# Optimization experiments

Measured on AMD Instinct MI355X. Metric: run time of the kernel, lower is better.

The kernel has to match this reference:

```python
import jax, jax.numpy as jnp
import numpy as np

B, C, H, W = 4, 512, 64, 64
C8 = C // 8


def setup_inputs() -> dict:
    key = jax.random.key(0)
    ks = jax.random.split(key, 5)
    s1 = 1.0 / np.sqrt(C)
    return {
        "feat_map": jax.random.normal(ks[0], (B, C, H, W), jnp.float32),
        "w1": jax.random.normal(ks[1], (C8, C), jnp.float32) * s1,
        "b1": jnp.zeros((C8,), jnp.float32),
        "w2": jax.random.normal(ks[2], (C8, C), jnp.float32) * s1,
        "b2": jnp.zeros((C8,), jnp.float32),
        "w3": jax.random.normal(ks[3], (C, C), jnp.float32) * s1,
        "b3": jnp.zeros((C,), jnp.float32),
        "gamma": jax.random.normal(ks[4], (1,), jnp.float32) * 0.1,
    }


def reference(feat_map, w1, b1, w2, b2, w3, b3, gamma):
    b, c, h, w = feat_map.shape
    n = h * w
    x = feat_map.reshape(b, c, n)  # [B,C,N]
    # 1x1 convs are channel-mixing GEMMs
    q = jnp.einsum('kc,bcn->bnk', w1, x) + b1[None, None, :]   # [B,N,C8]
    k = jnp.einsum('kc,bcn->bkn', w2, x) + b2[None, :, None]   # [B,C8,N]
    v = jnp.einsum('dc,bcn->bdn', w3, x) + b3[None, :, None]   # [B,C,N]
    relation = jnp.einsum('bik,bkj->bij', q, k)                # [B,N,N]
    attn = jax.nn.softmax(relation, axis=-1)                   # softmax over keys j
    # feat_refine[b,c,i] = sum_j v[b,c,j] * attn[b,i,j]
    refine = jnp.einsum('bdj,bij->bdi', v, attn)               # [B,C,N]
    out = gamma[0] * refine.reshape(b, c, h, w) + feat_map
    return out
```

## Files before the change

kernel.cpp:

```cpp
#include <hip/hip_runtime.h>
#include <hip/hip_bf16.h>

typedef __attribute__((ext_vector_type(8))) short bf16x8_t;
typedef __attribute__((ext_vector_type(4))) float f32x4_t;

#define B_   4
#define C_   512
#define N_   4096
#define NQK_ 128
#define NT_  128
#define NP_  64

typedef unsigned short ushort_t;

__device__ __forceinline__ ushort_t f2bf(float f) {
    union { float f; unsigned int u; } un; un.f = f;
    unsigned int r = un.u + 0x7FFF + ((un.u >> 16) & 1);
    return (ushort_t)(r >> 16);
}

__device__ __forceinline__ bf16x8_t load8(const ushort_t* p) {
    return *reinterpret_cast<const bf16x8_t*>(p);
}

__device__ __forceinline__ unsigned pk2(float lo, float hi) {
    return (unsigned)f2bf(lo) | ((unsigned)f2bf(hi) << 16);
}

#define GLL16(g, l) __builtin_amdgcn_global_load_lds( \
    (const __attribute__((address_space(1))) unsigned int*)(g), \
    (__attribute__((address_space(3))) unsigned int*)(l), 16, 0, 0)

__global__ __launch_bounds__(256) void transpose_cast_x(
        const float* __restrict__ x, ushort_t* __restrict__ Xt,
        const float* __restrict__ w1, const float* __restrict__ b1,
        const float* __restrict__ w2, const float* __restrict__ b2,
        const float* __restrict__ w3, const float* __restrict__ b3,
        ushort_t* __restrict__ Wb, float* __restrict__ bias_all) {
    if (blockIdx.z == 4) {
        int bid = blockIdx.y * 64 + blockIdx.x;
        int t0 = bid * 256 + threadIdx.x;
        for (int idx = t0; idx < 640 * 512 + 640; idx += 131072) {
            if (idx < 64 * 512) {
                Wb[idx] = f2bf(w1[idx]);
            } else if (idx < 128 * 512) {
                Wb[idx] = f2bf(w2[idx - 64 * 512]);
            } else if (idx < 640 * 512) {
                Wb[idx] = f2bf(w3[idx - 128 * 512]);
            } else {
                int i = idx - 640 * 512;
                bias_all[i] = (i < 64) ? b1[i] : (i < 128 ? b2[i - 64] : b3[i - 128]);
            }
        }
        return;
    }
    int b = blockIdx.z, c0 = blockIdx.y * 64, n0 = blockIdx.x * 64;
    int tid = threadIdx.x;
    __shared__ float t[64][65];
    const float* xb = x + ((size_t)b * C_ + c0) * N_ + n0;
    #pragma unroll
    for (int it = 0; it < 4; ++it) {
        int cl = it * 16 + (tid >> 4), nq = (tid & 15) * 4;
        const float4 v = *reinterpret_cast<const float4*>(xb + (size_t)cl * N_ + nq);
        t[cl][nq + 0] = v.x; t[cl][nq + 1] = v.y;
        t[cl][nq + 2] = v.z; t[cl][nq + 3] = v.w;
    }
    __syncthreads();
    #pragma unroll
    for (int it = 0; it < 4; ++it) {
        int nl = it * 16 + (tid >> 4), cq = (tid & 15) * 4;
        ushort4 o;
        o.x = f2bf(t[cq + 0][nl]); o.y = f2bf(t[cq + 1][nl]);
        o.z = f2bf(t[cq + 2][nl]); o.w = f2bf(t[cq + 3][nl]);
        *reinterpret_cast<ushort4*>(&Xt[((size_t)b * N_ + n0 + nl) * C_ + c0 + cq]) = o;
    }
}

__global__ __launch_bounds__(256) void gemm_qkv_kernel(
        const ushort_t* __restrict__ Xt, const ushort_t* __restrict__ Wb,
        const float* __restrict__ bias, ushort_t* __restrict__ QK,
        ushort_t* __restrict__ V) {
    __shared__ ushort_t Al[2][4096];
    __shared__ ushort_t Bl[2][4096];
    int sel = blockIdx.y;
    int n0 = blockIdx.x * 128;
    int tid = threadIdx.x;
    int l = tid & 63, w = tid >> 6;
    int wr = w >> 1, wc = w & 1;
    int lr = l & 15, lg = l >> 4;

    int m0 = 0, bV = 0;
    const ushort_t* asrc;
    const ushort_t* bsrc;
    if (sel < 4) {
        asrc = Xt + ((size_t)sel * N_ + n0) * 512;
        bsrc = Wb;
    } else {
        m0 = ((sel - 4) & 3) * 128;
        bV = (sel - 4) >> 2;
        asrc = Wb + (size_t)(128 + m0) * 512;
        bsrc = Xt + ((size_t)bV * N_ + n0) * 512;
    }
    const ushort_t* ast = asrc + (size_t)(l >> 2) * 512 + (l & 3) * 8;
    const ushort_t* bst = bsrc + (size_t)(l >> 2) * 512 + (l & 3) * 8;

#define STAGEK(BUF, K0)                                                        \
    {                                                                          \
        GLL16(ast + (size_t)(w * 32) * 512 + (K0),      &Al[BUF][w * 1024]);       \
        GLL16(ast + (size_t)(w * 32 + 16) * 512 + (K0), &Al[BUF][w * 1024 + 512]); \
        GLL16(bst + (size_t)(w * 32) * 512 + (K0),      &Bl[BUF][w * 1024]);       \
        GLL16(bst + (size_t)(w * 32 + 16) * 512 + (K0), &Bl[BUF][w * 1024 + 512]); \
    }

    f32x4_t acc[4][4] = {};
    STAGEK(0, 0)
    for (int i = 0; i < 16; ++i) {
        int cur = i & 1;
        if (i < 15) {
            STAGEK(cur ^ 1, (i + 1) * 32)
            asm volatile("s_waitcnt vmcnt(4)" ::: "memory");
        } else {
            asm volatile("s_waitcnt vmcnt(0)" ::: "memory");
        }
        asm volatile("" ::: "memory");
        __builtin_amdgcn_s_barrier();
        asm volatile("" ::: "memory");
        bf16x8_t a[4], b8[4];
        #pragma unroll
        for (int f = 0; f < 4; ++f) {
            a[f]  = load8(&Al[cur][(wr * 64 + f * 16 + lr) * 32 + lg * 8]);
            b8[f] = load8(&Bl[cur][(wc * 64 + f * 16 + lr) * 32 + lg * 8]);
        }
        #pragma unroll
        for (int fi = 0; fi < 4; ++fi)
            #pragma unroll
            for (int fj = 0; fj < 4; ++fj)
                acc[fi][fj] = __builtin_amdgcn_mfma_f32_16x16x32_bf16(
                    a[fi], b8[fj], acc[fi][fj], 0, 0, 0);
        asm volatile("" ::: "memory");
        __builtin_amdgcn_s_barrier();
        asm volatile("" ::: "memory");
    }
#undef STAGEK

    if (sel < 4) {
        #pragma unroll
        for (int fi = 0; fi < 4; ++fi)
            #pragma unroll
            for (int fj = 0; fj < 4; ++fj)
                #pragma unroll
                for (int r = 0; r < 4; ++r) {
                    int n = n0 + wr * 64 + fi * 16 + lg * 4 + r;
                    int col = wc * 64 + fj * 16 + lr;
                    QK[((size_t)sel * N_ + n) * NQK_ + col] = f2bf(acc[fi][fj][r] + bias[col]);
                }
    } else {
        #pragma unroll
        for (int fi = 0; fi < 4; ++fi)
            #pragma unroll
            for (int fj = 0; fj < 4; ++fj)
                #pragma unroll
                for (int r = 0; r < 4; ++r) {
                    int d = m0 + wr * 64 + fi * 16 + lg * 4 + r;
                    int n = n0 + wc * 64 + fj * 16 + lr;
                    V[((size_t)bV * C_ + d) * N_ + n] = f2bf(acc[fi][fj][r] + bias[128 + d]);
                }
    }
}

__global__ __launch_bounds__(768, 3) void attn_kernel(
        const ushort_t* __restrict__ QK, const ushort_t* __restrict__ V,
        const float* __restrict__ feat, const float* __restrict__ gamma,
        float* __restrict__ out) {
    __shared__ ushort_t Vl[3][16384];
    __shared__ ushort_t Kl3[3][4096];
    __shared__ ushort_t Pl[2][4096];
    __shared__ float    fl[2][128];
    __shared__ __align__(16) unsigned flagl[2][8];
    __shared__ float    invl[64];

    int bid = blockIdx.x;
    int lid = (bid & 7) * 32 + (bid >> 3);
    int b  = lid >> 6;
    int i0 = (lid & 63) * 64;

    int tid = threadIdx.x;
    int l = tid & 63, w = tid >> 6;
    int lr = l & 15, lg = l >> 4;
    int ds = (w >= 4) ? (w - 4) : 0;

    const ushort_t* QKb = QK + (size_t)b * N_ * NQK_;
    const ushort_t* Vb  = V  + (size_t)b * C_ * N_;

    bf16x8_t qf0 = {}, qf1 = {};
    const ushort_t* ksrc = nullptr;
    float mreg = -1e30f, ssum = 0.0f;
    const int maskk = (lr & 7) << 4;
    if (w < 4) {
        qf0 = load8(QKb + (size_t)(i0 + w * 16 + lr) * NQK_ + lg * 8);
        qf1 = load8(QKb + (size_t)(i0 + w * 16 + lr) * NQK_ + 32 + lg * 8);
        int p = w * 1024 + l * 16;
        int o = p ^ (((p >> 7) & 7) << 4);
        ksrc = QKb + (size_t)(o >> 7) * NQK_ + 64 + ((o & 127) >> 1);
    }

    int cst = (l & 7) ^ (l >> 3);
    const ushort_t* vsrc = Vb + (size_t)(ds * 64 + 2 * (l >> 3) + (cst >> 2)) * N_
                              + (cst & 3) * 8;
    int c2 = ((lr & 1) * 4 + lg) ^ (lr >> 1);
    const int vread = ds * 2048 + (lr >> 1) * 64 + c2 * 8;
    f32x4_t acc[4][4] = {};

    if (w < 4) {
        GLL16(ksrc,                         &Kl3[0][w * 512]);
        GLL16(ksrc + (size_t)1 * 32 * NQK_, &Kl3[0][2048 + w * 512]);
        GLL16(ksrc + (size_t)2 * 32 * NQK_, &Kl3[1][w * 512]);
        GLL16(ksrc + (size_t)3 * 32 * NQK_, &Kl3[1][2048 + w * 512]);
        asm volatile("s_waitcnt vmcnt(2)" ::: "memory");
    } else {
        #pragma unroll
        for (int h = 0; h < 4; ++h)
            GLL16(vsrc + (size_t)h * 16 * N_,      &Vl[0][ds * 2048 + h * 512]);
        #pragma unroll
        for (int h = 0; h < 4; ++h)
            GLL16(vsrc + (size_t)h * 16 * N_ + 32, &Vl[1][ds * 2048 + h * 512]);
        #pragma unroll
        for (int h = 0; h < 4; ++h)
            GLL16(vsrc + (size_t)h * 16 * N_ + 64, &Vl[2][ds * 2048 + h * 512]);
    }
    asm volatile("" ::: "memory");
    __builtin_amdgcn_s_barrier();
    asm volatile("" ::: "memory");

#define SOFTMAX_WRITE(SO0, SO1, PM, TT)                                        \
    {                                                                          \
        float pmax = fmaxf(fmaxf(fmaxf(SO0[0],SO0[1]), fmaxf(SO0[2],SO0[3])),  \
                           fmaxf(fmaxf(SO1[0],SO1[1]), fmaxf(SO1[2],SO1[3]))); \
        pmax = fmaxf(pmax, __shfl_xor(pmax, 16));                              \
        pmax = fmaxf(pmax, __shfl_xor(pmax, 32));                              \
        bool anyneed = __any(pmax > mreg + 8.0f);                              \
        if (anyneed) {                                                         \
            float mn = fmaxf(mreg, pmax);                                      \
            float f_ = __expf(mreg - mn);                                      \
            mreg = mn; ssum *= f_;                                             \
            if (lg == 0) fl[PM][(TT) * 64 + w * 16 + lr] = f_;                 \
        }                                                                      \
        if (l == 0) flagl[PM][(TT) * 4 + w] = anyneed ? 1u : 0u;               \
        float e00 = __expf(SO0[0]-mreg), e01 = __expf(SO0[1]-mreg);            \
        float e02 = __expf(SO0[2]-mreg), e03 = __expf(SO0[3]-mreg);            \
        float e10 = __expf(SO1[0]-mreg), e11 = __expf(SO1[1]-mreg);            \
        float e12 = __expf(SO1[2]-mreg), e13 = __expf(SO1[3]-mreg);            \
        ssum += (e00+e01)+(e02+e03)+(e10+e11)+(e12+e13);    \
        int lt = lr + (lg >> 1) * 16;                                          \
        uint2 w0v; w0v.x = pk2(e00, e01); w0v.y = pk2(e02, e03);               \
        uint2 w1v; w1v.x = pk2(e10, e11); w1v.y = pk2(e12, e13);               \
        *reinterpret_cast<uint2*>(&Pl[PM][(TT)*2048 + w*512 + lt*8 + (lg&1)*4]) = w0v; \
        *reinterpret_cast<uint2*>(&Pl[PM][(TT)*2048 + w*512 + (lt+32)*8 + (lg&1)*4]) = w1v; \
    }

#define PVSTEP(PB, TT, VB, STJ, DOSTAGE)                                       \
    {                                                                          \
        bf16x8_t vf[4];                                                        \
        _Pragma("unroll") for (int dt = 0; dt < 4; ++dt)                       \
            vf[dt] = load8(&Vl[VB][vread + dt * 512]);                         \
        asm volatile("s_waitcnt lgkmcnt(0)" ::: "memory");                     \
        if (DOSTAGE) {                                                         \
            const ushort_t* vsT = vsrc + (STJ) * 32;                           \
            _Pragma("unroll") for (int h = 0; h < 4; ++h)                      \
                GLL16(vsT + (size_t)h * 16 * N_, &Vl[VB][ds * 2048 + h * 512]); \
        }                                                                      \
        uint4 fv = *reinterpret_cast<const uint4*>(&flagl[PB][(TT) * 4]);      \
        if ((int)__builtin_amdgcn_readfirstlane(fv.x)) {                       \
            float fq = fl[PB][(TT) * 64 + lr];                                 \
            _Pragma("unroll") for (int dt = 0; dt < 4; ++dt) acc[dt][0] *= fq; \
        }                                                                      \
        if ((int)__builtin_amdgcn_readfirstlane(fv.y)) {                       \
            float fq = fl[PB][(TT) * 64 + 16 + lr];                            \
            _Pragma("unroll") for (int dt = 0; dt < 4; ++dt) acc[dt][1] *= fq; \
        }                                                                      \
        if ((int)__builtin_amdgcn_readfirstlane(fv.z)) {                       \
            float fq = fl[PB][(TT) * 64 + 32 + lr];                            \
            _Pragma("unroll") for (int dt = 0; dt < 4; ++dt) acc[dt][2] *= fq; \
        }                                                                      \
        if ((int)__builtin_amdgcn_readfirstlane(fv.w)) {                       \
            float fq = fl[PB][(TT) * 64 + 48 + lr];                            \
            _Pragma("unroll") for (int dt = 0; dt < 4; ++dt) acc[dt][3] *= fq; \
        }                                                                      \
        __builtin_amdgcn_s_setprio(1);                                         \
        _Pragma("unroll") for (int qt = 0; qt < 4; ++qt) {                     \
            bf16x8_t pa = load8(&Pl[PB][(TT) * 2048 + qt * 512 + l * 8]);      \
            _Pragma("unroll") for (int dt = 0; dt < 4; ++dt)                   \
                acc[dt][qt] = __builtin_amdgcn_mfma_f32_16x16x32_bf16(         \
                    vf[dt], pa, acc[dt][qt], 0, 0, 0);                         \
        }                                                                      \
        __builtin_amdgcn_s_setprio(0);                                         \
    }

    for (int p = 0; p < NP_; ++p) {
        int pb = p % 3;
        if (w < 4) {
            if (p + 2 < NP_) {
                int pn = pb + 2; if (pn >= 3) pn -= 3;
                GLL16(ksrc + (size_t)(2 * p + 4) * 32 * NQK_, &Kl3[pn][w * 512]);
                GLL16(ksrc + (size_t)(2 * p + 5) * 32 * NQK_, &Kl3[pn][2048 + w * 512]);
            }
            const ushort_t* kbp = &Kl3[pb][0];
            bf16x8_t kf00, kf01, kf10, kf11;
            { int o = (lr << 7) + (lg << 4);              kf00 = load8(kbp + ((o ^ maskk) >> 1)); }
            { int o = (lr << 7) + 64 + (lg << 4);         kf01 = load8(kbp + ((o ^ maskk) >> 1)); }
            { int o = ((16 + lr) << 7) + (lg << 4);       kf10 = load8(kbp + ((o ^ maskk) >> 1)); }
            { int o = ((16 + lr) << 7) + 64 + (lg << 4);  kf11 = load8(kbp + ((o ^ maskk) >> 1)); }
            f32x4_t s00 = {0.f,0.f,0.f,0.f}, s01 = {0.f,0.f,0.f,0.f};
            s00 = __builtin_amdgcn_mfma_f32_16x16x32_bf16(kf00, qf0, s00, 0,0,0);
            s00 = __builtin_amdgcn_mfma_f32_16x16x32_bf16(kf01, qf1, s00, 0,0,0);
            s01 = __builtin_amdgcn_mfma_f32_16x16x32_bf16(kf10, qf0, s01, 0,0,0);
            s01 = __builtin_amdgcn_mfma_f32_16x16x32_bf16(kf11, qf1, s01, 0,0,0);
            const ushort_t* kbq = kbp + 2048;
            bf16x8_t kg00, kg01, kg10, kg11;
            { int o = (lr << 7) + (lg << 4);              kg00 = load8(kbq + ((o ^ maskk) >> 1)); }
            { int o = (lr << 7) + 64 + (lg << 4);         kg01 = load8(kbq + ((o ^ maskk) >> 1)); }
            { int o = ((16 + lr) << 7) + (lg << 4);       kg10 = load8(kbq + ((o ^ maskk) >> 1)); }
            { int o = ((16 + lr) << 7) + 64 + (lg << 4);  kg11 = load8(kbq + ((o ^ maskk) >> 1)); }
            f32x4_t s10 = {0.f,0.f,0.f,0.f}, s11 = {0.f,0.f,0.f,0.f};
            s10 = __builtin_amdgcn_mfma_f32_16x16x32_bf16(kg00, qf0, s10, 0,0,0);
            s10 = __builtin_amdgcn_mfma_f32_16x16x32_bf16(kg01, qf1, s10, 0,0,0);
            s11 = __builtin_amdgcn_mfma_f32_16x16x32_bf16(kg10, qf0, s11, 0,0,0);
            s11 = __builtin_amdgcn_mfma_f32_16x16x32_bf16(kg11, qf1, s11, 0,0,0);
            int bank = p & 1;
            SOFTMAX_WRITE(s00, s01, bank, 0)
            SOFTMAX_WRITE(s10, s11, bank, 1)
            asm volatile("s_waitcnt vmcnt(2) lgkmcnt(0)" ::: "memory");
        } else {
            if (p >= 1) {
                int pbk = (p - 1) & 1;
                int j0 = 2 * p - 2, j1 = 2 * p - 1;
                PVSTEP(pbk, 0, j0 % 3, j0 + 3, (j0 + 3 < NT_))
                PVSTEP(pbk, 1, j1 % 3, j1 + 3, (j1 + 3 < NT_))
            }
            asm volatile("s_waitcnt vmcnt(4)" ::: "memory");
        }
        asm volatile("" ::: "memory");
        __builtin_amdgcn_s_barrier();
        asm volatile("" ::: "memory");
    }

    if (w < 4) {
        ssum += __shfl_xor(ssum, 16);
        ssum += __shfl_xor(ssum, 32);
        if (lg == 0) invl[w * 16 + lr] = 1.0f / ssum;
        asm volatile("s_waitcnt lgkmcnt(0)" ::: "memory");
    } else {
        asm volatile("s_waitcnt vmcnt(0)" ::: "memory");
    }
    asm volatile("" ::: "memory");
    __builtin_amdgcn_s_barrier();
    asm volatile("" ::: "memory");

    if (w >= 4) {
        PVSTEP(1, 0, 0, 0, false)
        PVSTEP(1, 1, 1, 0, false)
        asm volatile("s_waitcnt lgkmcnt(0)" ::: "memory");

        float g = gamma[0];
        float iq0 = invl[lr], iq1 = invl[16 + lr], iq2 = invl[32 + lr], iq3 = invl[48 + lr];
        #pragma unroll
        for (int dt = 0; dt < 4; ++dt) {
            #pragma unroll
            for (int r = 0; r < 4; ++r) {
                size_t row = ((size_t)b * C_ + ds * 64 + dt * 16 + lg * 4 + r) * N_;
                size_t i0r = row + i0;
                { size_t idx = i0r + lr;      out[idx] = g * acc[dt][0][r] * iq0 + feat[idx]; }
                { size_t idx = i0r + 16 + lr; out[idx] = g * acc[dt][1][r] * iq1 + feat[idx]; }
                { size_t idx = i0r + 32 + lr; out[idx] = g * acc[dt][2][r] * iq2 + feat[idx]; }
                { size_t idx = i0r + 48 + lr; out[idx] = g * acc[dt][3][r] * iq3 + feat[idx]; }
            }
        }
    }
#undef PVSTEP
#undef SOFTMAX_WRITE
}

extern "C" void kernel_launch(void* const* d_in, const int* in_sizes, int n_in,
                              void* d_out, int out_size, void* d_ws, size_t ws_size,
                              hipStream_t stream) {
    const float* feat  = (const float*)d_in[0];
    const float* w1    = (const float*)d_in[1];
    const float* b1    = (const float*)d_in[2];
    const float* w2    = (const float*)d_in[3];
    const float* b2    = (const float*)d_in[4];
    const float* w3    = (const float*)d_in[5];
    const float* b3    = (const float*)d_in[6];
    const float* gamma = (const float*)d_in[7];
    float* out = (float*)d_out;

    char* ws = (char*)d_ws;
    ushort_t* Xt      = (ushort_t*)(ws);
    ushort_t* Wb      = (ushort_t*)(ws + 16777216);
    float*    biasAll = (float*)   (ws + 17432576);
    ushort_t* QKp     = (ushort_t*)(ws + 17435136);
    ushort_t* Vp      = (ushort_t*)(ws + 21629440);
    if (ws_size < 38406656) return;

    hipLaunchKernelGGL(transpose_cast_x, dim3(64, 8, 5), dim3(256), 0, stream,
                       feat, Xt, w1, b1, w2, b2, w3, b3, Wb, biasAll);
    hipLaunchKernelGGL(gemm_qkv_kernel, dim3(32, 20), dim3(256), 0, stream,
                       Xt, Wb, biasAll, QKp, Vp);
    hipLaunchKernelGGL(attn_kernel, dim3(256), dim3(768), 0, stream,
                       QKp, Vp, feat, gamma, out);
}
```

Baseline: 139.7 us.

## Split PV work across softmax waves and shrink QKV GEMM tiles for more blocks

In the attention kernel, the four softmax waves now also take part in the P·V product: each covers 32 value channels (2 tiles), while the four PV waves drop from 64 to 48 channels (3 tiles). This spreads the MFMA load over all eight waves instead of leaving the softmax waves idle during PV, at the cost of extra vmcnt bookkeeping and more V staging traffic on the softmax waves. Separately, the QKV GEMM tile is halved along M (64 rows per block), raising the grid from 640 to 1280 blocks with a 1D index for better CU occupancy. The trade-off is lower per-block data reuse.

```diff
diff --git a/kernel.cpp b/kernel.cpp
--- a/kernel.cpp
+++ b/kernel.cpp
@@ -80,59 +80,60 @@
         const ushort_t* __restrict__ Xt, const ushort_t* __restrict__ Wb,
         const float* __restrict__ bias, ushort_t* __restrict__ QK,
         ushort_t* __restrict__ V) {
-    __shared__ ushort_t Al[2][4096];
+    __shared__ ushort_t Al[2][2048];
     __shared__ ushort_t Bl[2][4096];
-    int sel = blockIdx.y;
-    int n0 = blockIdx.x * 128;
+    int bid = blockIdx.x;
     int tid = threadIdx.x;
     int l = tid & 63, w = tid >> 6;
     int wr = w >> 1, wc = w & 1;
     int lr = l & 15, lg = l >> 4;
 
-    int m0 = 0, bV = 0;
+    int b, n0, d0 = 0;
+    bool isQK = (bid < 256);
     const ushort_t* asrc;
     const ushort_t* bsrc;
-    if (sel < 4) {
-        asrc = Xt + ((size_t)sel * N_ + n0) * 512;
+    if (isQK) {
+        b = bid >> 6; n0 = (bid & 63) * 64;
+        asrc = Xt + ((size_t)b * N_ + n0) * 512;
         bsrc = Wb;
     } else {
-        m0 = ((sel - 4) & 3) * 128;
-        bV = (sel - 4) >> 2;
-        asrc = Wb + (size_t)(128 + m0) * 512;
-        bsrc = Xt + ((size_t)bV * N_ + n0) * 512;
+        int v = bid - 256;
+        b = v >> 8; d0 = ((v >> 5) & 7) * 64; n0 = (v & 31) * 128;
+        asrc = Wb + (size_t)(128 + d0) * 512;
+        bsrc = Xt + ((size_t)b * N_ + n0) * 512;
     }
     const ushort_t* ast = asrc + (size_t)(l >> 2) * 512 + (l & 3) * 8;
     const ushort_t* bst = bsrc + (size_t)(l >> 2) * 512 + (l & 3) * 8;
 
-#define STAGEK(BUF, K0)                                                        \
-    {                                                                          \
-        GLL16(ast + (size_t)(w * 32) * 512 + (K0),      &Al[BUF][w * 1024]);       \
-        GLL16(ast + (size_t)(w * 32 + 16) * 512 + (K0), &Al[BUF][w * 1024 + 512]); \
-        GLL16(bst + (size_t)(w * 32) * 512 + (K0),      &Bl[BUF][w * 1024]);       \
+#define STAGEK(BUF, K0)                                                          \
+    {                                                                            \
+        GLL16(ast + (size_t)(w * 16) * 512 + (K0),      &Al[BUF][w * 512]);      \
+        GLL16(bst + (size_t)(w * 32) * 512 + (K0),      &Bl[BUF][w * 1024]);     \
         GLL16(bst + (size_t)(w * 32 + 16) * 512 + (K0), &Bl[BUF][w * 1024 + 512]); \
     }
 
-    f32x4_t acc[4][4] = {};
+    f32x4_t acc[2][4] = {};
     STAGEK(0, 0)
     for (int i = 0; i < 16; ++i) {
         int cur = i & 1;
         if (i < 15) {
             STAGEK(cur ^ 1, (i + 1) * 32)
-            asm volatile("s_waitcnt vmcnt(4)" ::: "memory");
+            asm volatile("s_waitcnt vmcnt(3)" ::: "memory");
         } else {
             asm volatile("s_waitcnt vmcnt(0)" ::: "memory");
         }
         asm volatile("" ::: "memory");
         __builtin_amdgcn_s_barrier();
         asm volatile("" ::: "memory");
-        bf16x8_t a[4], b8[4];
-        #pragma unroll
-        for (int f = 0; f < 4; ++f) {
-            a[f]  = load8(&Al[cur][(wr * 64 + f * 16 + lr) * 32 + lg * 8]);
+        bf16x8_t a[2], b8[4];
+        #pragma unroll
+        for (int f = 0; f < 2; ++f)
+            a[f]  = load8(&Al[cur][(wr * 32 + f * 16 + lr) * 32 + lg * 8]);
+        #pragma unroll
+        for (int f = 0; f < 4; ++f)
             b8[f] = load8(&Bl[cur][(wc * 64 + f * 16 + lr) * 32 + lg * 8]);
-        }
-        #pragma unroll
-        for (int fi = 0; fi < 4; ++fi)
+        #pragma unroll
+        for (int fi = 0; fi < 2; ++fi)
             #pragma unroll
             for (int fj = 0; fj < 4; ++fj)
                 acc[fi][fj] = __builtin_amdgcn_mfma_f32_16x16x32_bf16(
@@ -143,27 +144,27 @@
     }
 #undef STAGEK
 
-    if (sel < 4) {
-        #pragma unroll
-        for (int fi = 0; fi < 4; ++fi)
+    if (isQK) {
+        #pragma unroll
+        for (int fi = 0; fi < 2; ++fi)
             #pragma unroll
             for (int fj = 0; fj < 4; ++fj)
                 #pragma unroll
                 for (int r = 0; r < 4; ++r) {
-                    int n = n0 + wr * 64 + fi * 16 + lg * 4 + r;
+                    int n = n0 + wr * 32 + fi * 16 + lg * 4 + r;
                     int col = wc * 64 + fj * 16 + lr;
-                    QK[((size_t)sel * N_ + n) * NQK_ + col] = f2bf(acc[fi][fj][r] + bias[col]);
+                    QK[((size_t)b * N_ + n) * NQK_ + col] = f2bf(acc[fi][fj][r] + bias[col]);
                 }
     } else {
         #pragma unroll
-        for (int fi = 0; fi < 4; ++fi)
+        for (int fi = 0; fi < 2; ++fi)
             #pragma unroll
             for (int fj = 0; fj < 4; ++fj)
                 #pragma unroll
                 for (int r = 0; r < 4; ++r) {
-                    int d = m0 + wr * 64 + fi * 16 + lg * 4 + r;
+                    int d = d0 + wr * 32 + fi * 16 + lg * 4 + r;
                     int n = n0 + wc * 64 + fj * 16 + lr;
-                    V[((size_t)bV * C_ + d) * N_ + n] = f2bf(acc[fi][fj][r] + bias[128 + d]);
+                    V[((size_t)b * C_ + d) * N_ + n] = f2bf(acc[fi][fj][r] + bias[128 + d]);
                 }
     }
 }
@@ -187,7 +188,8 @@
     int tid = threadIdx.x;
     int l = tid & 63, w = tid >> 6;
     int lr = l & 15, lg = l >> 4;
-    int ds = (w >= 4) ? (w - 4) : 0;
+
+    int chbase = (w < 4) ? (384 + w * 32) : ((w - 4) * 48);
 
     const ushort_t* QKb = QK + (size_t)b * N_ * NQK_;
     const ushort_t* Vb  = V  + (size_t)b * C_ * N_;
@@ -205,28 +207,30 @@
     }
 
     int cst = (l & 7) ^ (l >> 3);
-    const ushort_t* vsrc = Vb + (size_t)(ds * 64 + 2 * (l >> 3) + (cst >> 2)) * N_
+    const ushort_t* vsrc = Vb + (size_t)(chbase + 2 * (l >> 3) + (cst >> 2)) * N_
                               + (cst & 3) * 8;
     int c2 = ((lr & 1) * 4 + lg) ^ (lr >> 1);
-    const int vread = ds * 2048 + (lr >> 1) * 64 + c2 * 8;
-    f32x4_t acc[4][4] = {};
+    const int vread = chbase * 32 + (lr >> 1) * 64 + c2 * 8;
+    f32x4_t acc[3][4] = {};
 
     if (w < 4) {
         GLL16(ksrc,                         &Kl3[0][w * 512]);
         GLL16(ksrc + (size_t)1 * 32 * NQK_, &Kl3[0][2048 + w * 512]);
         GLL16(ksrc + (size_t)2 * 32 * NQK_, &Kl3[1][w * 512]);
         GLL16(ksrc + (size_t)3 * 32 * NQK_, &Kl3[1][2048 + w * 512]);
-        asm volatile("s_waitcnt vmcnt(2)" ::: "memory");
+        #pragma unroll
+        for (int j = 0; j < 3; ++j)
+            #pragma unroll
+            for (int h = 0; h < 2; ++h)
+                GLL16(vsrc + (size_t)h * 16 * N_ + j * 32,
+                      &Vl[j][chbase * 32 + h * 512]);
     } else {
         #pragma unroll
-        for (int h = 0; h < 4; ++h)
-            GLL16(vsrc + (size_t)h * 16 * N_,      &Vl[0][ds * 2048 + h * 512]);
-        #pragma unroll
-        for (int h = 0; h < 4; ++h)
-            GLL16(vsrc + (size_t)h * 16 * N_ + 32, &Vl[1][ds * 2048 + h * 512]);
-        #pragma unroll
-        for (int h = 0; h < 4; ++h)
-            GLL16(vsrc + (size_t)h * 16 * N_ + 64, &Vl[2][ds * 2048 + h * 512]);
+        for (int j = 0; j < 3; ++j)
+            #pragma unroll
+            for (int h = 0; h < 3; ++h)
+                GLL16(vsrc + (size_t)h * 16 * N_ + j * 32,
+                      &Vl[j][chbase * 32 + h * 512]);
     }
     asm volatile("" ::: "memory");
     __builtin_amdgcn_s_barrier();
@@ -258,38 +262,38 @@
         *reinterpret_cast<uint2*>(&Pl[PM][(TT)*2048 + w*512 + (lt+32)*8 + (lg&1)*4]) = w1v; \
     }
 
-#define PVSTEP(PB, TT, VB, STJ, DOSTAGE)                                       \
+#define PVSTEP(PB, TT, VB, STJ, DOSTAGE, DTN, NGL)                             \
     {                                                                          \
-        bf16x8_t vf[4];                                                        \
-        _Pragma("unroll") for (int dt = 0; dt < 4; ++dt)                       \
+        bf16x8_t vf[3];                                                        \
+        _Pragma("unroll") for (int dt = 0; dt < (DTN); ++dt)                   \
             vf[dt] = load8(&Vl[VB][vread + dt * 512]);                         \
         asm volatile("s_waitcnt lgkmcnt(0)" ::: "memory");                     \
         if (DOSTAGE) {                                                         \
             const ushort_t* vsT = vsrc + (STJ) * 32;                           \
-            _Pragma("unroll") for (int h = 0; h < 4; ++h)                      \
-                GLL16(vsT + (size_t)h * 16 * N_, &Vl[VB][ds * 2048 + h * 512]); \
+            _Pragma("unroll") for (int h = 0; h < (NGL); ++h)                  \
+                GLL16(vsT + (size_t)h * 16 * N_, &Vl[VB][chbase * 32 + h * 512]); \
         }                                                                      \
         uint4 fv = *reinterpret_cast<const uint4*>(&flagl[PB][(TT) * 4]);      \
         if ((int)__builtin_amdgcn_readfirstlane(fv.x)) {                       \
             float fq = fl[PB][(TT) * 64 + lr];                                 \
-            _Pragma("unroll") for (int dt = 0; dt < 4; ++dt) acc[dt][0] *= fq; \
+            _Pragma("unroll") for (int dt = 0; dt < (DTN); ++dt) acc[dt][0] *= fq; \
         }                                                                      \
         if ((int)__builtin_amdgcn_readfirstlane(fv.y)) {                       \
             float fq = fl[PB][(TT) * 64 + 16 + lr];                            \
-            _Pragma("unroll") for (int dt = 0; dt < 4; ++dt) acc[dt][1] *= fq; \
+            _Pragma("unroll") for (int dt = 0; dt < (DTN); ++dt) acc[dt][1] *= fq; \
         }                                                                      \
         if ((int)__builtin_amdgcn_readfirstlane(fv.z)) {                       \
             float fq = fl[PB][(TT) * 64 + 32 + lr];                            \
-            _Pragma("unroll") for (int dt = 0; dt < 4; ++dt) acc[dt][2] *= fq; \
+            _Pragma("unroll") for (int dt = 0; dt < (DTN); ++dt) acc[dt][2] *= fq; \
         }                                                                      \
         if ((int)__builtin_amdgcn_readfirstlane(fv.w)) {                       \
             float fq = fl[PB][(TT) * 64 + 48 + lr];                            \
-            _Pragma("unroll") for (int dt = 0; dt < 4; ++dt) acc[dt][3] *= fq; \
+            _Pragma("unroll") for (int dt = 0; dt < (DTN); ++dt) acc[dt][3] *= fq; \
         }                                                                      \
         __builtin_amdgcn_s_setprio(1);                                         \
         _Pragma("unroll") for (int qt = 0; qt < 4; ++qt) {                     \
             bf16x8_t pa = load8(&Pl[PB][(TT) * 2048 + qt * 512 + l * 8]);      \
-            _Pragma("unroll") for (int dt = 0; dt < 4; ++dt)                   \
+            _Pragma("unroll") for (int dt = 0; dt < (DTN); ++dt)               \
                 acc[dt][qt] = __builtin_amdgcn_mfma_f32_16x16x32_bf16(         \
                     vf[dt], pa, acc[dt][qt], 0, 0, 0);                         \
         }                                                                      \
@@ -299,6 +303,7 @@
     for (int p = 0; p < NP_; ++p) {
         int pb = p % 3;
         if (w < 4) {
+            asm volatile("s_waitcnt vmcnt(6)" ::: "memory");
             if (p + 2 < NP_) {
                 int pn = pb + 2; if (pn >= 3) pn -= 3;
                 GLL16(ksrc + (size_t)(2 * p + 4) * 32 * NQK_, &Kl3[pn][w * 512]);
@@ -329,15 +334,25 @@
             int bank = p & 1;
             SOFTMAX_WRITE(s00, s01, bank, 0)
             SOFTMAX_WRITE(s10, s11, bank, 1)
-            asm volatile("s_waitcnt vmcnt(2) lgkmcnt(0)" ::: "memory");
+            if (p >= 1) {
+                int pbk = (p - 1) & 1;
+                int j0 = 2 * p - 2, j1 = 2 * p - 1;
+                if (p < 62) { asm volatile("s_waitcnt vmcnt(4)" ::: "memory"); }
+                else        { asm volatile("s_waitcnt vmcnt(2)" ::: "memory"); }
+                PVSTEP(pbk, 0, j0 % 3, j0 + 3, (j0 + 3 < NT_), 2, 2)
+                if (p < 62) { asm volatile("s_waitcnt vmcnt(4)" ::: "memory"); }
+                else        { asm volatile("s_waitcnt vmcnt(2)" ::: "memory"); }
+                PVSTEP(pbk, 1, j1 % 3, j1 + 3, (j1 + 3 < NT_), 2, 2)
+            }
+            asm volatile("s_waitcnt lgkmcnt(0)" ::: "memory");
         } else {
             if (p >= 1) {
                 int pbk = (p - 1) & 1;
                 int j0 = 2 * p - 2, j1 = 2 * p - 1;
-                PVSTEP(pbk, 0, j0 % 3, j0 + 3, (j0 + 3 < NT_))
-                PVSTEP(pbk, 1, j1 % 3, j1 + 3, (j1 + 3 < NT_))
+                PVSTEP(pbk, 0, j0 % 3, j0 + 3, (j0 + 3 < NT_), 3, 3)
+                PVSTEP(pbk, 1, j1 % 3, j1 + 3, (j1 + 3 < NT_), 3, 3)
             }
-            asm volatile("s_waitcnt vmcnt(4)" ::: "memory");
+            asm volatile("s_waitcnt vmcnt(3)" ::: "memory");
         }
         asm volatile("" ::: "memory");
         __builtin_amdgcn_s_barrier();
@@ -348,7 +363,7 @@
         ssum += __shfl_xor(ssum, 16);
         ssum += __shfl_xor(ssum, 32);
         if (lg == 0) invl[w * 16 + lr] = 1.0f / ssum;
-        asm volatile("s_waitcnt lgkmcnt(0)" ::: "memory");
+        asm volatile("s_waitcnt vmcnt(0) lgkmcnt(0)" ::: "memory");
     } else {
         asm volatile("s_waitcnt vmcnt(0)" ::: "memory");
     }
@@ -356,18 +371,23 @@
     __builtin_amdgcn_s_barrier();
     asm volatile("" ::: "memory");
 
-    if (w >= 4) {
-        PVSTEP(1, 0, 0, 0, false)
-        PVSTEP(1, 1, 1, 0, false)
+    {
+        if (w < 4) {
+            PVSTEP(1, 0, 0, 0, false, 2, 2)
+            PVSTEP(1, 1, 1, 0, false, 2, 2)
+        } else {
+            PVSTEP(1, 0, 0, 0, false, 3, 3)
+            PVSTEP(1, 1, 1, 0, false, 3, 3)
+        }
         asm volatile("s_waitcnt lgkmcnt(0)" ::: "memory");
 
         float g = gamma[0];
         float iq0 = invl[lr], iq1 = invl[16 + lr], iq2 = invl[32 + lr], iq3 = invl[48 + lr];
-        #pragma unroll
-        for (int dt = 0; dt < 4; ++dt) {
+        int ndt = (w < 4) ? 2 : 3;
+        for (int dt = 0; dt < ndt; ++dt) {
             #pragma unroll
             for (int r = 0; r < 4; ++r) {
-                size_t row = ((size_t)b * C_ + ds * 64 + dt * 16 + lg * 4 + r) * N_;
+                size_t row = ((size_t)b * C_ + chbase + dt * 16 + lg * 4 + r) * N_;
                 size_t i0r = row + i0;
                 { size_t idx = i0r + lr;      out[idx] = g * acc[dt][0][r] * iq0 + feat[idx]; }
                 { size_t idx = i0r + 16 + lr; out[idx] = g * acc[dt][1][r] * iq1 + feat[idx]; }
@@ -403,7 +423,7 @@
 
     hipLaunchKernelGGL(transpose_cast_x, dim3(64, 8, 5), dim3(256), 0, stream,
                        feat, Xt, w1, b1, w2, b2, w3, b3, Wb, biasAll);
-    hipLaunchKernelGGL(gemm_qkv_kernel, dim3(32, 20), dim3(256), 0, stream,
+    hipLaunchKernelGGL(gemm_qkv_kernel, dim3(1280), dim3(256), 0, stream,
                        Xt, Wb, biasAll, QKp, Vp);
     hipLaunchKernelGGL(attn_kernel, dim3(256), dim3(768), 0, stream,
                        QKp, Vp, feat, gamma, out);
```

Result: slower. 535.6 us (+283.4%).
